# Kernel optimization log

Measured on AMD Instinct MI355X. Metric: run time of the kernel, lower is better.

## Reference

```python
import jax, jax.numpy as jnp
import numpy as np

N, F, H, C = 50000, 128, 4, 32  # nodes, in-features, heads, per-head dim
E = 800000
D = H * C  # concat output dim = 128


def _tconv(x, src, dst, ea, Wq, bq, Wk, bk, Wv, bv, We, Ws, bs):
    # PyG TransformerConv (concat=True, root_weight=True, beta=False, eval mode)
    n = x.shape[0]
    q = (x @ Wq + bq).reshape(n, H, C)
    k = (x @ Wk + bk).reshape(n, H, C)
    v = (x @ Wv + bv).reshape(n, H, C)
    e = (ea @ We).reshape(-1, H, C)            # edge embedding [E,H,C]
    kj = k[src] + e                            # gathered keys + edge emb
    alpha = jnp.einsum('ehc,ehc->eh', q[dst], kj) / jnp.sqrt(jnp.float32(C))
    amax = jax.ops.segment_max(alpha, dst, num_segments=n)
    ex = jnp.exp(alpha - amax[dst])
    denom = jax.ops.segment_sum(ex, dst, num_segments=n)
    w = ex / (denom[dst] + 1e-16)              # segment softmax over in-edges
    msg = (v[src] + e) * w[:, :, None]
    out = jax.ops.segment_sum(msg, dst, num_segments=n).reshape(n, D)
    return out + x @ Ws + bs                   # skip connection


def setup_inputs() -> dict:
    key = jax.random.key(0)
    ks = jax.random.split(key, 24)
    s = lambda i, shape, scale: jax.random.normal(ks[i], shape, dtype=jnp.float32) * scale
    inp = {
        'x': s(0, (N, F), 1.0),
        'edge_index': jax.random.randint(ks[1], (2, E), 0, N),
        'edge_attr': s(2, (E,), 1.0),
        # layer 1 (in = F)
        'Wq1': s(3, (F, D), 1.0 / np.sqrt(F)), 'bq1': jnp.zeros((D,), jnp.float32),
        'Wk1': s(4, (F, D), 1.0 / np.sqrt(F)), 'bk1': jnp.zeros((D,), jnp.float32),
        'Wv1': s(5, (F, D), 1.0 / np.sqrt(F)), 'bv1': jnp.zeros((D,), jnp.float32),
        'We1': s(6, (1, D), 1.0),
        'Ws1': s(7, (F, D), 1.0 / np.sqrt(F)), 'bs1': jnp.zeros((D,), jnp.float32),
        # layer 2 (in = D)
        'Wq2': s(8, (D, D), 1.0 / np.sqrt(D)), 'bq2': jnp.zeros((D,), jnp.float32),
        'Wk2': s(9, (D, D), 1.0 / np.sqrt(D)), 'bk2': jnp.zeros((D,), jnp.float32),
        'Wv2': s(10, (D, D), 1.0 / np.sqrt(D)), 'bv2': jnp.zeros((D,), jnp.float32),
        'We2': s(11, (1, D), 1.0),
        'Ws2': s(12, (D, D), 1.0 / np.sqrt(D)), 'bs2': jnp.zeros((D,), jnp.float32),
    }
    return inp


def reference(x, edge_index, edge_attr,
              Wq1, bq1, Wk1, bk1, Wv1, bv1, We1, Ws1, bs1,
              Wq2, bq2, Wk2, bk2, Wv2, bv2, We2, Ws2, bs2):
    src, dst = edge_index[0], edge_index[1]
    ea = edge_attr.reshape(-1, 1)
    h = _tconv(x, src, dst, ea, Wq1, bq1, Wk1, bk1, Wv1, bv1, We1, Ws1, bs1)
    h = jax.nn.relu(h)  # dropout is identity in eval mode
    h = _tconv(h, src, dst, ea, Wq2, bq2, Wk2, bk2, Wv2, bv2, We2, Ws2, bs2)
    return jax.nn.relu(h)
```

## Files before the change

kernel.cpp:

```cpp
#include <hip/hip_runtime.h>


#define TPB 256

typedef __attribute__((ext_vector_type(8))) short short8v;
typedef __attribute__((ext_vector_type(8))) unsigned short ushort8v;
typedef __attribute__((ext_vector_type(16))) float f32x16;

__device__ __forceinline__ unsigned short f2bf(float f) {
    unsigned u = __float_as_uint(f);
    u = (u + 0x7FFFu + ((u >> 16) & 1u)) >> 16;
    return (unsigned short)u;
}
__device__ __forceinline__ float bf2f(unsigned short s) {
    return __uint_as_float((unsigned)s << 16);
}
__device__ __forceinline__ float exp2_hw(float x) {
    float r;
    asm("v_exp_f32 %0, %1" : "=v"(r) : "v"(x));
    return r;
}

__global__ void __launch_bounds__(TPB) prep_cvt_k(
    const float* __restrict__ Wq1, const float* __restrict__ Wk1,
    const float* __restrict__ Wv1, const float* __restrict__ Ws1,
    const float* __restrict__ Wq2, const float* __restrict__ Wk2,
    const float* __restrict__ Wv2, const float* __restrict__ Ws2,
    unsigned short* __restrict__ pack,
    const float* __restrict__ x, unsigned short* __restrict__ xb, int n4)
{
    if (blockIdx.x < 512) {
        int i = blockIdx.x * TPB + threadIdx.x;
        int j = i & 7, lane = (i >> 3) & 63, t = (i >> 9) & 7, nc = (i >> 12) & 3, g = (i >> 14) & 7;
        const float* Wt[8] = {Wq1, Wk1, Wv1, Ws1, Wq2, Wk2, Wv2, Ws2};
        const float* W = Wt[g];
        int kk = t * 16 + (lane >> 5) * 8 + j;
        int nn = nc * 32 + (lane & 31);
        pack[i] = f2bf(W[kk * 128 + nn]);
    } else {
        int i = (blockIdx.x - 512) * TPB + threadIdx.x;
        if (i >= n4) return;
        float4 v = *(const float4*)(x + (size_t)i * 4);
        ushort4 o;
        o.x = f2bf(v.x); o.y = f2bf(v.y); o.z = f2bf(v.z); o.w = f2bf(v.w);
        *(ushort4*)(xb + (size_t)i * 4) = o;
    }
}

__global__ void __launch_bounds__(TPB) gemm_mfma_k(
    const unsigned short* __restrict__ A, int M,
    const unsigned short* __restrict__ pack,
    const float* __restrict__ bq, const float* __restrict__ bk,
    const float* __restrict__ bv, const float* __restrict__ bs,
    unsigned short* __restrict__ oq, unsigned short* __restrict__ okv,
    unsigned short* __restrict__ os)
{
    const int g = blockIdx.y;
    const int row0 = blockIdx.x * 128;
    const int wv = threadIdx.x >> 6;
    const int lane = threadIdx.x & 63;
    const int rbase = row0 + wv * 32;
    const int arow = rbase + (lane & 31);
    const int kh = (lane >> 5) * 8;

    const short8v z8 = {0, 0, 0, 0, 0, 0, 0, 0};
    short8v a[8];
    if (arow < M) {
        const unsigned short* Ap = A + (size_t)arow * 128 + kh;
#pragma unroll
        for (int t = 0; t < 8; ++t) a[t] = *(const short8v*)(Ap + t * 16);
    } else {
#pragma unroll
        for (int t = 0; t < 8; ++t) a[t] = z8;
    }

    f32x16 acc[4];
#pragma unroll
    for (int nc = 0; nc < 4; ++nc)
#pragma unroll
        for (int r = 0; r < 16; ++r) acc[nc][r] = 0.f;

    const unsigned short* bp = pack + (size_t)g * 16384;
#pragma unroll
    for (int nc = 0; nc < 4; ++nc) {
#pragma unroll
        for (int t = 0; t < 8; ++t) {
            short8v b = *(const short8v*)(bp + (nc * 8 + t) * 512 + lane * 8);
            acc[nc] = __builtin_amdgcn_mfma_f32_32x32x16_bf16(a[t], b, acc[nc], 0, 0, 0);
        }
    }

    const float* bias = g == 0 ? bq : (g == 1 ? bk : (g == 2 ? bv : bs));
    const int col = lane & 31;
    const int rb2 = rbase + 4 * (lane >> 5);
    unsigned short* out = g == 0 ? oq : (g == 3 ? os : okv);
    const int stride = (g == 1 || g == 2) ? 256 : 128;
    const int goff = g == 2 ? 128 : 0;
#pragma unroll
    for (int nc = 0; nc < 4; ++nc) {
        float bb = bias[nc * 32 + col];
#pragma unroll
        for (int r = 0; r < 16; ++r) {
            int row = rb2 + (r & 3) + 8 * (r >> 2);
            if (row < M)
                out[(size_t)row * stride + goff + nc * 32 + col] = f2bf(acc[nc][r] + bb);
        }
    }
}

__global__ void __launch_bounds__(TPB) hist_k(const int* __restrict__ dst,
                                              int* __restrict__ deg, int E)
{
    int e = blockIdx.x * TPB + threadIdx.x;
    if (e < E) atomicAdd(&deg[dst[e]], 1);
}

__global__ void __launch_bounds__(TPB) scan_a_k(const int* __restrict__ deg, int n,
                                                int* __restrict__ incl,
                                                int* __restrict__ bsum,
                                                int* __restrict__ bcnt, int nb,
                                                int* __restrict__ rank)
{
    __shared__ int ts[TPB];
    __shared__ int lhist[64];
    if (threadIdx.x < 64) lhist[threadIdx.x] = 0;
    const int base = blockIdx.x * 1024;
    int vals[4], s = 0;
#pragma unroll
    for (int j = 0; j < 4; ++j) {
        int i = base + threadIdx.x * 4 + j;
        vals[j] = (i < n) ? deg[i] : 0;
        s += vals[j];
    }
    ts[threadIdx.x] = s;
    __syncthreads();
#pragma unroll
    for (int j = 0; j < 4; ++j) {
        int i = base + threadIdx.x * 4 + j;
        if (i < n) {
            int bin = 63 - min(vals[j], 63);
            rank[i] = atomicAdd(&lhist[bin], 1);
        }
    }
    for (int off = 1; off < TPB; off <<= 1) {
        int u = (threadIdx.x >= off) ? ts[threadIdx.x - off] : 0;
        __syncthreads();
        ts[threadIdx.x] += u;
        __syncthreads();
    }
    int run = ts[threadIdx.x] - s;
#pragma unroll
    for (int j = 0; j < 4; ++j) {
        run += vals[j];
        int i = base + threadIdx.x * 4 + j;
        if (i < n) incl[i] = run;
    }
    if (threadIdx.x == TPB - 1) bsum[blockIdx.x] = ts[TPB - 1];
    __syncthreads();
    if (threadIdx.x < 64) bcnt[threadIdx.x * nb + blockIdx.x] = lhist[threadIdx.x];
}

__global__ void __launch_bounds__(TPB) scan_b_k(int* __restrict__ bsum, int nb,
                                                int* __restrict__ bcnt)
{
    __shared__ int ts[TPB];
    const int t = threadIdx.x;
    int v = (t < nb) ? bsum[t] : 0;
    ts[t] = v;
    __syncthreads();
    for (int off = 1; off < TPB; off <<= 1) {
        int u = (t >= off) ? ts[t - off] : 0;
        __syncthreads();
        ts[t] += u;
        __syncthreads();
    }
    if (t < nb) bsum[t] = ts[t] - v;
    __syncthreads();

    const int total = 64 * nb;
    const int C = (total + TPB - 1) / TPB;
    int loc[32];
    int s = 0;
    for (int j = 0; j < C; ++j) {
        int i = t * C + j;
        loc[j] = (i < total) ? bcnt[i] : 0;
        s += loc[j];
    }
    __syncthreads();
    ts[t] = s;
    __syncthreads();
    for (int off = 1; off < TPB; off <<= 1) {
        int u = (t >= off) ? ts[t - off] : 0;
        __syncthreads();
        ts[t] += u;
        __syncthreads();
    }
    int run = ts[t] - s;
    for (int j = 0; j < C; ++j) {
        int i = t * C + j;
        if (i < total) bcnt[i] = run;
        run += loc[j];
    }
}

__global__ void __launch_bounds__(TPB) finalize_k(const int* __restrict__ incl,
                                                  const int* __restrict__ deg,
                                                  const int* __restrict__ bsum, int n,
                                                  int* __restrict__ row_ptr,
                                                  int* __restrict__ cursor,
                                                  const int* __restrict__ bcnt, int nb,
                                                  const int* __restrict__ rank,
                                                  int* __restrict__ perm)
{
    const int base = blockIdx.x * 1024;
    const int boff = bsum[blockIdx.x];
#pragma unroll
    for (int j = 0; j < 4; ++j) {
        int i = base + threadIdx.x * 4 + j;
        if (i < n) {
            int dg = deg[i];
            int iv = incl[i] + boff;
            row_ptr[i] = iv - dg;
            cursor[i] = iv - dg;
            if (i == n - 1) row_ptr[n] = iv;
            int bin = 63 - min(dg, 63);
            perm[bcnt[bin * nb + blockIdx.x] + rank[i]] = i;
        }
    }
}

__global__ void __launch_bounds__(TPB) scatter_k(
    const int* __restrict__ src, const int* __restrict__ dst,
    const float* __restrict__ ea, int* __restrict__ cursor,
    unsigned* __restrict__ csr_pack, int E)
{
    int e = blockIdx.x * TPB + threadIdx.x;
    if (e >= E) return;
    int pos = atomicAdd(&cursor[dst[e]], 1);
    csr_pack[pos] = ((unsigned)f2bf(ea[e]) << 16) | (unsigned)src[e];
}

template <bool BF16OUT>
__global__ void __launch_bounds__(TPB) node_attn_k(
    const unsigned short* __restrict__ q, const unsigned short* __restrict__ kv,
    const unsigned short* __restrict__ skip, const float* __restrict__ We,
    const int* __restrict__ row_ptr, const unsigned* __restrict__ csr_pack,
    const int* __restrict__ perm,
    void* __restrict__ outp, int n)
{
    const int slot = blockIdx.x * 16 + (threadIdx.x >> 4);
    if (slot >= n) return;
    const int node = perm[slot];
    const int l16 = threadIdx.x & 15;
    const int c8 = l16 * 8;

    const float C2 = 0.17677669529663687f * 1.44269504088896f;

    float we8[8], qv[8];
    {
        float4 wlo = *(const float4*)(We + c8);
        float4 whi = *(const float4*)(We + c8 + 4);
        we8[0] = wlo.x; we8[1] = wlo.y; we8[2] = wlo.z; we8[3] = wlo.w;
        we8[4] = whi.x; we8[5] = whi.y; we8[6] = whi.z; we8[7] = whi.w;
        ushort8v qu = *(const ushort8v*)(q + (size_t)node * 128 + c8);
#pragma unroll
        for (int i = 0; i < 8; ++i) qv[i] = bf2f((unsigned short)qu[i]) * C2;
    }

    float qwe = 0.f;
#pragma unroll
    for (int i = 0; i < 8; ++i) qwe = fmaf(qv[i], we8[i], qwe);
    qwe += __shfl_xor(qwe, 1);
    qwe += __shfl_xor(qwe, 2);

    const int p0 = row_ptr[node], p1 = row_ptr[node + 1];

    float m = -3.4e38f, l = 0.f, sae = 0.f;
    float acc[8];
#pragma unroll
    for (int i = 0; i < 8; ++i) acc[i] = 0.f;

    for (int j = p0; j < p1; j += 8) {
        const int last = p1 - 1;
        unsigned pr[8];
#pragma unroll
        for (int t = 0; t < 8; ++t) pr[t] = csr_pack[min(j + t, last)];

        ushort8v ku[8], vu[8];
#pragma unroll
        for (int t = 0; t < 8; ++t) {
            const unsigned short* b = kv + (pr[t] & 0xFFFFu) * 256u + c8;
            ku[t] = *(const ushort8v*)b;
            vu[t] = *(const ushort8v*)(b + 128);
        }

        float d[8];
#pragma unroll
        for (int t = 0; t < 8; ++t) {
            float dd = 0.f;
#pragma unroll
            for (int i = 0; i < 8; ++i)
                dd = fmaf(bf2f((unsigned short)ku[t][i]), qv[i], dd);
            dd += __shfl_xor(dd, 1);
            dd += __shfl_xor(dd, 2);
            d[t] = dd;
        }

        float eav[8], al[8];
#pragma unroll
        for (int t = 0; t < 8; ++t) {
            eav[t] = bf2f((unsigned short)(pr[t] >> 16));
            al[t] = (t == 0 || j + t < p1) ? fmaf(eav[t], qwe, d[t]) : -3.4e38f;
        }

        float mn = m;
#pragma unroll
        for (int t = 0; t < 8; ++t) mn = fmaxf(mn, al[t]);
        float sc = exp2_hw(m - mn);
        float pe[8];
#pragma unroll
        for (int t = 0; t < 8; ++t) pe[t] = exp2_hw(al[t] - mn);

        float ls = 0.f, ss = 0.f;
#pragma unroll
        for (int t = 0; t < 8; ++t) { ls += pe[t]; ss = fmaf(pe[t], eav[t], ss); }
        l = fmaf(l, sc, ls);
        sae = fmaf(sae, sc, ss);
#pragma unroll
        for (int i = 0; i < 8; ++i) {
            float mv = 0.f;
#pragma unroll
            for (int t = 0; t < 8; ++t)
                mv = fmaf(pe[t], bf2f((unsigned short)vu[t][i]), mv);
            acc[i] = fmaf(acc[i], sc, mv);
        }
        m = mn;
    }

    float inv = 1.f / (l + 1e-16f);
    ushort8v sku = *(const ushort8v*)(skip + (size_t)node * 128 + c8);
    float o[8];
#pragma unroll
    for (int i = 0; i < 8; ++i)
        o[i] = fmaxf(fmaf(fmaf(sae, we8[i], acc[i]), inv,
                          bf2f((unsigned short)sku[i])), 0.f);

    if (BF16OUT) {
        ushort8v ov;
#pragma unroll
        for (int i = 0; i < 8; ++i) ov[i] = f2bf(o[i]);
        *(ushort8v*)((unsigned short*)outp + (size_t)node * 128 + c8) = ov;
    } else {
        float* op = (float*)outp + (size_t)node * 128 + c8;
        *(float4*)op = make_float4(o[0], o[1], o[2], o[3]);
        *(float4*)(op + 4) = make_float4(o[4], o[5], o[6], o[7]);
    }
}

extern "C" void kernel_launch(void* const* d_in, const int* in_sizes, int n_in,
                              void* d_out, int out_size, void* d_ws, size_t ws_size,
                              hipStream_t stream)
{
    const float* x   = (const float*)d_in[0];
    const int*   ei  = (const int*)d_in[1];
    const float* ea  = (const float*)d_in[2];
    const float* Wq1 = (const float*)d_in[3];  const float* bq1 = (const float*)d_in[4];
    const float* Wk1 = (const float*)d_in[5];  const float* bk1 = (const float*)d_in[6];
    const float* Wv1 = (const float*)d_in[7];  const float* bv1 = (const float*)d_in[8];
    const float* We1 = (const float*)d_in[9];
    const float* Ws1 = (const float*)d_in[10]; const float* bs1 = (const float*)d_in[11];
    const float* Wq2 = (const float*)d_in[12]; const float* bq2 = (const float*)d_in[13];
    const float* Wk2 = (const float*)d_in[14]; const float* bk2 = (const float*)d_in[15];
    const float* Wv2 = (const float*)d_in[16]; const float* bv2 = (const float*)d_in[17];
    const float* We2 = (const float*)d_in[18];
    const float* Ws2 = (const float*)d_in[19]; const float* bs2 = (const float*)d_in[20];

    const int N = in_sizes[0] / 128;
    const int E = in_sizes[1] / 2;
    const int* src = ei;
    const int* dst = ei + E;
    float* outf = (float*)d_out;

    const int nb = (N + 1023) / 1024;

    unsigned short* q  = (unsigned short*)d_ws;
    unsigned short* kv = q + (size_t)N * 128;
    unsigned short* s  = kv + (size_t)N * 256;
    unsigned short* xb = s + (size_t)N * 128;
    unsigned short* pk = xb + (size_t)N * 128;
    int*   row_ptr = (int*)(pk + 131072);
    int*   deg     = row_ptr + (N + 1);
    int*   incl    = deg + N;
    int*   cursor  = incl + N;
    int*   rank    = cursor + N;
    int*   bsum    = rank + N;
    int*   bcnt    = bsum + 256;
    int*   perm    = bcnt + 64 * nb;
    unsigned* csr_pack = (unsigned*)(perm + N);

    const int gE   = (E + TPB - 1) / TPB;
    const int gN16 = (N + 15) / 16;
    const int n4   = N * 128 / 4;
    const int gPC  = 512 + (n4 + TPB - 1) / TPB;
    const int gG   = (N + 127) / 128;
    const dim3 gGd(gG, 4);

    hipMemsetAsync(deg, 0, (size_t)N * sizeof(int), stream);
    hist_k<<<gE, TPB, 0, stream>>>(dst, deg, E);
    scan_a_k<<<nb, TPB, 0, stream>>>(deg, N, incl, bsum, bcnt, nb, rank);
    scan_b_k<<<1, TPB, 0, stream>>>(bsum, nb, bcnt);
    finalize_k<<<nb, TPB, 0, stream>>>(incl, deg, bsum, N, row_ptr, cursor,
                                       bcnt, nb, rank, perm);
    scatter_k<<<gE, TPB, 0, stream>>>(src, dst, ea, cursor, csr_pack, E);

    prep_cvt_k<<<gPC, TPB, 0, stream>>>(Wq1, Wk1, Wv1, Ws1, Wq2, Wk2, Wv2, Ws2,
                                        pk, x, xb, n4);

    gemm_mfma_k<<<gGd, TPB, 0, stream>>>(xb, N, pk, bq1, bk1, bv1, bs1, q, kv, s);
    node_attn_k<true><<<gN16, TPB, 0, stream>>>(q, kv, s, We1, row_ptr, csr_pack,
                                                perm, xb, N);
    gemm_mfma_k<<<gGd, TPB, 0, stream>>>(xb, N, pk + 65536, bq2, bk2, bv2, bs2,
                                         q, kv, s);
    node_attn_k<false><<<gN16, TPB, 0, stream>>>(q, kv, s, We2, row_ptr, csr_pack,
                                                 perm, outf, N);
}
```

Baseline: 303.0 us.

## Merge histogram with prep, scatter with layer-1 GEMM, and remap GEMM blocks

The degree histogram is now launched together with weight packing and x conversion in one kernel, and the CSR scatter shares a launch with the layer-1 QKVS GEMM. Both fusions use block-index ranges to pick the work. This cuts two kernel launches and lets independent work run concurrently on the GPU. The GEMM grid also becomes 1D with a swizzled slot-to-tile mapping (slot&7 times pxi), intended to spread the four weight groups and row tiles across XCDs for better L2 locality. The mixed kernels may carry the register footprint of the GEMM path, which could lower occupancy for the atomic scatter and histogram blocks.

```diff
diff --git a/kernel.cpp b/kernel.cpp
--- a/kernel.cpp
+++ b/kernel.cpp
@@ -21,7 +21,74 @@
     return r;
 }
 
-__global__ void __launch_bounds__(TPB) prep_cvt_k(
+__device__ __forceinline__ void gemm_body(
+    int slot, int pxi, int nrt,
+    const unsigned short* __restrict__ A, int M,
+    const unsigned short* __restrict__ pack,
+    const float* __restrict__ bq, const float* __restrict__ bk,
+    const float* __restrict__ bv, const float* __restrict__ bs,
+    unsigned short* __restrict__ oq, unsigned short* __restrict__ okv,
+    unsigned short* __restrict__ os)
+{
+    const int x = slot & 7, jj = slot >> 3;
+    const int idx = x * pxi + jj;
+    if (idx >= nrt * 4) return;
+    const int g = idx & 3;
+    const int row0 = (idx >> 2) * 128;
+
+    const int wv = threadIdx.x >> 6;
+    const int lane = threadIdx.x & 63;
+    const int rbase = row0 + wv * 32;
+    const int arow = rbase + (lane & 31);
+    const int kh = (lane >> 5) * 8;
+
+    const short8v z8 = {0, 0, 0, 0, 0, 0, 0, 0};
+    short8v a[8];
+    if (arow < M) {
+        const unsigned short* Ap = A + (size_t)arow * 128 + kh;
+#pragma unroll
+        for (int t = 0; t < 8; ++t) a[t] = *(const short8v*)(Ap + t * 16);
+    } else {
+#pragma unroll
+        for (int t = 0; t < 8; ++t) a[t] = z8;
+    }
+
+    f32x16 acc[4];
+#pragma unroll
+    for (int nc = 0; nc < 4; ++nc)
+#pragma unroll
+        for (int r = 0; r < 16; ++r) acc[nc][r] = 0.f;
+
+    const unsigned short* bp = pack + (size_t)g * 16384;
+#pragma unroll
+    for (int nc = 0; nc < 4; ++nc) {
+#pragma unroll
+        for (int t = 0; t < 8; ++t) {
+            short8v b = *(const short8v*)(bp + (nc * 8 + t) * 512 + lane * 8);
+            acc[nc] = __builtin_amdgcn_mfma_f32_32x32x16_bf16(a[t], b, acc[nc], 0, 0, 0);
+        }
+    }
+
+    const float* bias = g == 0 ? bq : (g == 1 ? bk : (g == 2 ? bv : bs));
+    const int col = lane & 31;
+    const int rb2 = rbase + 4 * (lane >> 5);
+    unsigned short* out = g == 0 ? oq : (g == 3 ? os : okv);
+    const int stride = (g == 1 || g == 2) ? 256 : 128;
+    const int goff = g == 2 ? 128 : 0;
+#pragma unroll
+    for (int nc = 0; nc < 4; ++nc) {
+        float bb = bias[nc * 32 + col];
+#pragma unroll
+        for (int r = 0; r < 16; ++r) {
+            int row = rb2 + (r & 3) + 8 * (r >> 2);
+            if (row < M)
+                out[(size_t)row * stride + goff + nc * 32 + col] = f2bf(acc[nc][r] + bb);
+        }
+    }
+}
+
+__global__ void __launch_bounds__(TPB) hist_prep_cvt_k(
+    const int* __restrict__ dst, int* __restrict__ deg, int E, int gE,
     const float* __restrict__ Wq1, const float* __restrict__ Wk1,
     const float* __restrict__ Wv1, const float* __restrict__ Ws1,
     const float* __restrict__ Wq2, const float* __restrict__ Wk2,
@@ -29,8 +96,11 @@
     unsigned short* __restrict__ pack,
     const float* __restrict__ x, unsigned short* __restrict__ xb, int n4)
 {
-    if (blockIdx.x < 512) {
-        int i = blockIdx.x * TPB + threadIdx.x;
+    if (blockIdx.x < (unsigned)gE) {
+        int e = blockIdx.x * TPB + threadIdx.x;
+        if (e < E) atomicAdd(&deg[dst[e]], 1);
+    } else if (blockIdx.x < (unsigned)(gE + 512)) {
+        int i = (blockIdx.x - gE) * TPB + threadIdx.x;
         int j = i & 7, lane = (i >> 3) & 63, t = (i >> 9) & 7, nc = (i >> 12) & 3, g = (i >> 14) & 7;
         const float* Wt[8] = {Wq1, Wk1, Wv1, Ws1, Wq2, Wk2, Wv2, Ws2};
         const float* W = Wt[g];
@@ -38,81 +108,13 @@
         int nn = nc * 32 + (lane & 31);
         pack[i] = f2bf(W[kk * 128 + nn]);
     } else {
-        int i = (blockIdx.x - 512) * TPB + threadIdx.x;
+        int i = (blockIdx.x - gE - 512) * TPB + threadIdx.x;
         if (i >= n4) return;
         float4 v = *(const float4*)(x + (size_t)i * 4);
         ushort4 o;
         o.x = f2bf(v.x); o.y = f2bf(v.y); o.z = f2bf(v.z); o.w = f2bf(v.w);
         *(ushort4*)(xb + (size_t)i * 4) = o;
     }
-}
-
-__global__ void __launch_bounds__(TPB) gemm_mfma_k(
-    const unsigned short* __restrict__ A, int M,
-    const unsigned short* __restrict__ pack,
-    const float* __restrict__ bq, const float* __restrict__ bk,
-    const float* __restrict__ bv, const float* __restrict__ bs,
-    unsigned short* __restrict__ oq, unsigned short* __restrict__ okv,
-    unsigned short* __restrict__ os)
-{
-    const int g = blockIdx.y;
-    const int row0 = blockIdx.x * 128;
-    const int wv = threadIdx.x >> 6;
-    const int lane = threadIdx.x & 63;
-    const int rbase = row0 + wv * 32;
-    const int arow = rbase + (lane & 31);
-    const int kh = (lane >> 5) * 8;
-
-    const short8v z8 = {0, 0, 0, 0, 0, 0, 0, 0};
-    short8v a[8];
-    if (arow < M) {
-        const unsigned short* Ap = A + (size_t)arow * 128 + kh;
-#pragma unroll
-        for (int t = 0; t < 8; ++t) a[t] = *(const short8v*)(Ap + t * 16);
-    } else {
-#pragma unroll
-        for (int t = 0; t < 8; ++t) a[t] = z8;
-    }
-
-    f32x16 acc[4];
-#pragma unroll
-    for (int nc = 0; nc < 4; ++nc)
-#pragma unroll
-        for (int r = 0; r < 16; ++r) acc[nc][r] = 0.f;
-
-    const unsigned short* bp = pack + (size_t)g * 16384;
-#pragma unroll
-    for (int nc = 0; nc < 4; ++nc) {
-#pragma unroll
-        for (int t = 0; t < 8; ++t) {
-            short8v b = *(const short8v*)(bp + (nc * 8 + t) * 512 + lane * 8);
-            acc[nc] = __builtin_amdgcn_mfma_f32_32x32x16_bf16(a[t], b, acc[nc], 0, 0, 0);
-        }
-    }
-
-    const float* bias = g == 0 ? bq : (g == 1 ? bk : (g == 2 ? bv : bs));
-    const int col = lane & 31;
-    const int rb2 = rbase + 4 * (lane >> 5);
-    unsigned short* out = g == 0 ? oq : (g == 3 ? os : okv);
-    const int stride = (g == 1 || g == 2) ? 256 : 128;
-    const int goff = g == 2 ? 128 : 0;
-#pragma unroll
-    for (int nc = 0; nc < 4; ++nc) {
-        float bb = bias[nc * 32 + col];
-#pragma unroll
-        for (int r = 0; r < 16; ++r) {
-            int row = rb2 + (r & 3) + 8 * (r >> 2);
-            if (row < M)
-                out[(size_t)row * stride + goff + nc * 32 + col] = f2bf(acc[nc][r] + bb);
-        }
-    }
-}
-
-__global__ void __launch_bounds__(TPB) hist_k(const int* __restrict__ dst,
-                                              int* __restrict__ deg, int E)
-{
-    int e = blockIdx.x * TPB + threadIdx.x;
-    if (e < E) atomicAdd(&deg[dst[e]], 1);
 }
 
 __global__ void __launch_bounds__(TPB) scan_a_k(const int* __restrict__ deg, int n,
@@ -229,15 +231,38 @@
     }
 }
 
-__global__ void __launch_bounds__(TPB) scatter_k(
+__global__ void __launch_bounds__(TPB) scatter_gemm_k(
     const int* __restrict__ src, const int* __restrict__ dst,
     const float* __restrict__ ea, int* __restrict__ cursor,
-    unsigned* __restrict__ csr_pack, int E)
-{
-    int e = blockIdx.x * TPB + threadIdx.x;
-    if (e >= E) return;
-    int pos = atomicAdd(&cursor[dst[e]], 1);
-    csr_pack[pos] = ((unsigned)f2bf(ea[e]) << 16) | (unsigned)src[e];
+    unsigned* __restrict__ csr_pack, int E, int gE,
+    int pxi, int nrt,
+    const unsigned short* __restrict__ A, int M,
+    const unsigned short* __restrict__ pack,
+    const float* __restrict__ bq, const float* __restrict__ bk,
+    const float* __restrict__ bv, const float* __restrict__ bs,
+    unsigned short* __restrict__ oq, unsigned short* __restrict__ okv,
+    unsigned short* __restrict__ os)
+{
+    if (blockIdx.x < (unsigned)gE) {
+        int e = blockIdx.x * TPB + threadIdx.x;
+        if (e >= E) return;
+        int pos = atomicAdd(&cursor[dst[e]], 1);
+        csr_pack[pos] = ((unsigned)f2bf(ea[e]) << 16) | (unsigned)src[e];
+    } else {
+        gemm_body(blockIdx.x - gE, pxi, nrt, A, M, pack, bq, bk, bv, bs, oq, okv, os);
+    }
+}
+
+__global__ void __launch_bounds__(TPB) gemm_k(
+    int pxi, int nrt,
+    const unsigned short* __restrict__ A, int M,
+    const unsigned short* __restrict__ pack,
+    const float* __restrict__ bq, const float* __restrict__ bk,
+    const float* __restrict__ bv, const float* __restrict__ bs,
+    unsigned short* __restrict__ oq, unsigned short* __restrict__ okv,
+    unsigned short* __restrict__ os)
+{
+    gemm_body(blockIdx.x, pxi, nrt, A, M, pack, bq, bk, bv, bs, oq, okv, os);
 }
 
 template <bool BF16OUT>
@@ -401,26 +426,25 @@
     const int gE   = (E + TPB - 1) / TPB;
     const int gN16 = (N + 15) / 16;
     const int n4   = N * 128 / 4;
-    const int gPC  = 512 + (n4 + TPB - 1) / TPB;
-    const int gG   = (N + 127) / 128;
-    const dim3 gGd(gG, 4);
+    const int gCv  = (n4 + TPB - 1) / TPB;
+    const int nrt  = (N + 127) / 128;
+    const int pxi  = ((nrt + 7) / 8) * 4;
+    const int gGm  = 8 * pxi;
 
     hipMemsetAsync(deg, 0, (size_t)N * sizeof(int), stream);
-    hist_k<<<gE, TPB, 0, stream>>>(dst, deg, E);
+    hist_prep_cvt_k<<<gE + 512 + gCv, TPB, 0, stream>>>(
+        dst, deg, E, gE, Wq1, Wk1, Wv1, Ws1, Wq2, Wk2, Wv2, Ws2, pk, x, xb, n4);
     scan_a_k<<<nb, TPB, 0, stream>>>(deg, N, incl, bsum, bcnt, nb, rank);
     scan_b_k<<<1, TPB, 0, stream>>>(bsum, nb, bcnt);
     finalize_k<<<nb, TPB, 0, stream>>>(incl, deg, bsum, N, row_ptr, cursor,
                                        bcnt, nb, rank, perm);
-    scatter_k<<<gE, TPB, 0, stream>>>(src, dst, ea, cursor, csr_pack, E);
-
-    prep_cvt_k<<<gPC, TPB, 0, stream>>>(Wq1, Wk1, Wv1, Ws1, Wq2, Wk2, Wv2, Ws2,
-                                        pk, x, xb, n4);
-
-    gemm_mfma_k<<<gGd, TPB, 0, stream>>>(xb, N, pk, bq1, bk1, bv1, bs1, q, kv, s);
+    scatter_gemm_k<<<gE + gGm, TPB, 0, stream>>>(
+        src, dst, ea, cursor, csr_pack, E, gE, pxi, nrt,
+        xb, N, pk, bq1, bk1, bv1, bs1, q, kv, s);
     node_attn_k<true><<<gN16, TPB, 0, stream>>>(q, kv, s, We1, row_ptr, csr_pack,
                                                 perm, xb, N);
-    gemm_mfma_k<<<gGd, TPB, 0, stream>>>(xb, N, pk + 65536, bq2, bk2, bv2, bs2,
-                                         q, kv, s);
+    gemm_k<<<gGm, TPB, 0, stream>>>(pxi, nrt, xb, N, pk + 65536,
+                                    bq2, bk2, bv2, bs2, q, kv, s);
     node_attn_k<false><<<gN16, TPB, 0, stream>>>(q, kv, s, We2, row_ptr, csr_pack,
                                                  perm, outf, N);
 }
```

Result: faster. 295.5 us (-2.5%).
